# Optimization experiments

Measured on AMD Instinct MI355X. Metric: run time of the kernel, lower is better.

## Reference

```python
import jax, jax.numpy as jnp
import numpy as np

H = 1024      # hidden_dim
S = 32768     # seq_len


def setup_inputs() -> dict:
    key = jax.random.key(0)
    k1, k2, k3, k4, k5 = jax.random.split(key, 5)
    hidden = jax.random.normal(k1, (1, 2 * H), dtype=jnp.float32)
    encoder_output = jax.random.normal(k2, (S, H), dtype=jnp.float32)
    # nn.Linear default init scale ~ 1/sqrt(fan_in)
    attn_w = jax.random.normal(k3, (H, 3 * H), dtype=jnp.float32) / np.sqrt(3 * H)
    attn_b = jax.random.normal(k4, (H,), dtype=jnp.float32) / np.sqrt(3 * H)
    v_w = jax.random.normal(k5, (1, H), dtype=jnp.float32) / np.sqrt(H)
    return {"hidden": hidden, "encoder_output": encoder_output,
            "attn_w": attn_w, "attn_b": attn_b, "v_w": v_w}


def reference(hidden, encoder_output, attn_w, attn_b, v_w):
    seq_len = encoder_output.shape[0]
    h_rep = jnp.broadcast_to(hidden, (seq_len, hidden.shape[1]))  # repeat(seq_len, 1)
    cat = jnp.concatenate([h_rep, encoder_output], axis=1)        # [S, 3H]
    energy = jnp.tanh(cat @ attn_w.T + attn_b)                    # [S, H]
    attention = (energy @ v_w.T).squeeze()                        # [S]
    return jax.nn.softmax(attention, axis=0)
```

## Files before the change

kernel.cpp:

```cpp
#include <hip/hip_runtime.h>
#include <hip/hip_bf16.h>

#define H  1024
#define S  32768
#define H2 2048
#define H3 3072

typedef __attribute__((ext_vector_type(8))) short bf16x8;
typedef __attribute__((ext_vector_type(4))) float f32x4;

__device__ __forceinline__ unsigned short f2bf(float f) {
    unsigned u = __float_as_uint(f);
    u += 0x7fffu + ((u >> 16) & 1u);
    return (unsigned short)(u >> 16);
}

__device__ __forceinline__ unsigned cvt_pk(float lo, float hi) {
    __hip_bfloat162 h = __float22bfloat162_rn(make_float2(lo, hi));
    unsigned u;
    __builtin_memcpy(&u, &h, 4);
    return u;
}

__device__ __forceinline__ float tanh_fast(float x) {
    float e = __expf(2.0f * x);
    return 1.0f - 2.0f / (e + 1.0f);
}

__device__ __forceinline__ void async_copy16(const void* g, void* l) {
    __builtin_amdgcn_global_load_lds(
        (const __attribute__((address_space(1))) unsigned int*)g,
        (__attribute__((address_space(3))) unsigned int*)l,
        16, 0, 0);
}

__global__ void prep_all(const float* __restrict__ enc, const float* __restrict__ attn_w,
                         const float* __restrict__ attn_b, const float* __restrict__ hidden,
                         unsigned short* __restrict__ ebf, unsigned short* __restrict__ w2b,
                         float* __restrict__ dvec, float* __restrict__ logits, int do_enc) {
    int b = blockIdx.x;
    if (b < 32) {
        ((float4*)logits)[b * 256 + threadIdx.x] = (float4){0.f, 0.f, 0.f, 0.f};
        return;
    }
    b -= 32;
    if (do_enc) {
        if (b < 32768) {
            size_t idx4 = (size_t)b * 256 + threadIdx.x;
            float4 f = ((const float4*)enc)[idx4];
            ushort4 u;
            u.x = f2bf(f.x); u.y = f2bf(f.y); u.z = f2bf(f.z); u.w = f2bf(f.w);
            ((ushort4*)ebf)[idx4] = u;
            return;
        }
        b -= 32768;
    }
    if (b < 1024) {
        int idx4 = b * 256 + threadIdx.x;
        int n = idx4 >> 8;
        int c = (idx4 & 255) * 4;
        float4 f = *(const float4*)(attn_w + (size_t)n * H3 + H2 + c);
        ushort4 u;
        u.x = f2bf(f.x); u.y = f2bf(f.y); u.z = f2bf(f.z); u.w = f2bf(f.w);
        *(ushort4*)(w2b + (size_t)n * H + c) = u;
        return;
    }
    b -= 1024;
    int wv = threadIdx.x >> 6, lane = threadIdx.x & 63;
    int row = b * 4 + wv;
    const float* wrow = attn_w + (size_t)row * H3;
    float s = 0.f;
    #pragma unroll
    for (int j = 0; j < 32; ++j) {
        int k = lane + j * 64;
        s += wrow[k] * hidden[k];
    }
    #pragma unroll
    for (int m = 1; m <= 32; m <<= 1) s += __shfl_xor(s, m);
    if (lane == 0) dvec[row] = s + attn_b[row];
}

__device__ __forceinline__ void epilogue(const f32x4 acc[4][4], const float* __restrict__ dvec,
                                         const float* __restrict__ vw, float* __restrict__ logits,
                                         int rowBlock, int colBlock, int waveM, int waveN,
                                         int quad, int l16) {
    float rowsum[4][4];
    #pragma unroll
    for (int mi = 0; mi < 4; ++mi)
        #pragma unroll
        for (int r = 0; r < 4; ++r) rowsum[mi][r] = 0.f;

    #pragma unroll
    for (int ni = 0; ni < 4; ++ni) {
        int colg = colBlock * 128 + waveN * 64 + ni * 16 + l16;
        float dv = dvec[colg];
        float vv = vw[colg];
        #pragma unroll
        for (int mi = 0; mi < 4; ++mi)
            #pragma unroll
            for (int r = 0; r < 4; ++r)
                rowsum[mi][r] += tanh_fast(acc[mi][ni][r] + dv) * vv;
    }

    #pragma unroll
    for (int mi = 0; mi < 4; ++mi)
        #pragma unroll
        for (int r = 0; r < 4; ++r) {
            float s = rowsum[mi][r];
            s += __shfl_xor(s, 1);
            s += __shfl_xor(s, 2);
            s += __shfl_xor(s, 4);
            s += __shfl_xor(s, 8);
            rowsum[mi][r] = s;
        }

    if (l16 == 0) {
        int rbase = rowBlock * 128 + waveM * 64 + quad * 4;
        #pragma unroll
        for (int mi = 0; mi < 4; ++mi)
            #pragma unroll
            for (int r = 0; r < 4; ++r)
                atomicAdd(&logits[rbase + mi * 16 + r], rowsum[mi][r]);
    }
}

__global__ __launch_bounds__(256, 2) void attn_gemm_fast(
        const unsigned short* __restrict__ ebf, const unsigned short* __restrict__ w2b,
        const float* __restrict__ dvec, const float* __restrict__ vw,
        float* __restrict__ logits) {
    __shared__ unsigned short Atile[128 * 64];
    __shared__ unsigned short Btile[128 * 64];

    const int tid = threadIdx.x;
    const int rowBlock = blockIdx.x & 255;
    const int colBlock = blockIdx.x >> 8;

    const int lane = tid & 63;
    const int wv = tid >> 6;
    const int waveM = wv >> 1, waveN = wv & 1;
    const int quad = lane >> 4, l16 = lane & 15;

    f32x4 acc[4][4];
    #pragma unroll
    for (int mi = 0; mi < 4; ++mi)
        #pragma unroll
        for (int ni = 0; ni < 4; ++ni)
            acc[mi][ni] = (f32x4){0.f, 0.f, 0.f, 0.f};

    const size_t aRow0 = (size_t)(rowBlock * 128) * H;
    const size_t bRow0 = (size_t)(colBlock * 128) * H;

    int srow[4], sk[4];
    #pragma unroll
    for (int p = 0; p < 4; ++p) {
        int c = p * 256 + tid;
        srow[p] = c >> 3;
        sk[p] = ((c & 7) ^ (srow[p] & 7)) * 8;
    }

    for (int kt = 0; kt < 16; ++kt) {
        const int k0 = kt * 64;

        #pragma unroll
        for (int p = 0; p < 4; ++p) {
            int c = p * 256 + tid;
            async_copy16(ebf + aRow0 + (size_t)srow[p] * H + k0 + sk[p],
                         (char*)Atile + (size_t)c * 16);
        }
        #pragma unroll
        for (int p = 0; p < 4; ++p) {
            int c = p * 256 + tid;
            async_copy16(w2b + bRow0 + (size_t)srow[p] * H + k0 + sk[p],
                         (char*)Btile + (size_t)c * 16);
        }

        __syncthreads();

        #pragma unroll
        for (int kk = 0; kk < 2; ++kk) {
            const int slot = ((kk * 4 + quad) ^ (l16 & 7)) * 16;
            bf16x8 af[4], bfr[4];
            #pragma unroll
            for (int i = 0; i < 4; ++i) {
                int ar = waveM * 64 + i * 16 + l16;
                int br = waveN * 64 + i * 16 + l16;
                af[i]  = *(const bf16x8*)((const char*)Atile + ar * 128 + slot);
                bfr[i] = *(const bf16x8*)((const char*)Btile + br * 128 + slot);
            }
            #pragma unroll
            for (int mi = 0; mi < 4; ++mi)
                #pragma unroll
                for (int ni = 0; ni < 4; ++ni)
                    acc[mi][ni] = __builtin_amdgcn_mfma_f32_16x16x32_bf16(
                        af[mi], bfr[ni], acc[mi][ni], 0, 0, 0);
        }

        __syncthreads();
    }

    epilogue(acc, dvec, vw, logits, rowBlock, colBlock, waveM, waveN, quad, l16);
}

__global__ __launch_bounds__(256, 2) void attn_gemm_fb(
        const float* __restrict__ enc, const unsigned short* __restrict__ w2b,
        const float* __restrict__ dvec, const float* __restrict__ vw,
        float* __restrict__ logits) {
    __shared__ unsigned short Atile[128 * 32];
    __shared__ unsigned short Btile[128 * 32];

    const int tid = threadIdx.x;
    const int rowBlock = blockIdx.x & 255;
    const int colBlock = blockIdx.x >> 8;

    const int lane = tid & 63;
    const int wv = tid >> 6;
    const int waveM = wv >> 1, waveN = wv & 1;
    const int quad = lane >> 4, l16 = lane & 15;

    f32x4 acc[4][4];
    #pragma unroll
    for (int mi = 0; mi < 4; ++mi)
        #pragma unroll
        for (int ni = 0; ni < 4; ++ni)
            acc[mi][ni] = (f32x4){0.f, 0.f, 0.f, 0.f};

    const int arow = tid >> 3;
    const int akc  = (tid & 7) * 4;
    const size_t encRowBase = (size_t)(rowBlock * 128) * H;

    const unsigned short* Abase = Atile + (waveM * 64 + l16) * 32 + quad * 8;
    const unsigned short* Bbase = Btile + (waveN * 64 + l16) * 32 + quad * 8;

    for (int kt = 0; kt < 32; ++kt) {
        const int k0 = kt * 32;
        #pragma unroll
        for (int p = 0; p < 2; ++p) {
            int c = p * 256 + tid;
            int n = c >> 2, kk = (c & 3) * 8;
            async_copy16(w2b + (size_t)(colBlock * 128 + n) * H + k0 + kk,
                         (char*)Btile + (size_t)c * 16);
        }
        float4 av[4];
        #pragma unroll
        for (int p = 0; p < 4; ++p)
            av[p] = *(const float4*)(enc + encRowBase + (size_t)(arow + p * 32) * H + k0 + akc);
        #pragma unroll
        for (int p = 0; p < 4; ++p) {
            uint2 u;
            u.x = cvt_pk(av[p].x, av[p].y);
            u.y = cvt_pk(av[p].z, av[p].w);
            *(uint2*)(Atile + (arow + p * 32) * 32 + akc) = u;
        }

        __syncthreads();

        bf16x8 af[4], bfr[4];
        #pragma unroll
        for (int i = 0; i < 4; ++i) {
            af[i]  = *(const bf16x8*)(Abase + i * 16 * 32);
            bfr[i] = *(const bf16x8*)(Bbase + i * 16 * 32);
        }
        #pragma unroll
        for (int mi = 0; mi < 4; ++mi)
            #pragma unroll
            for (int ni = 0; ni < 4; ++ni)
                acc[mi][ni] = __builtin_amdgcn_mfma_f32_16x16x32_bf16(
                    af[mi], bfr[ni], acc[mi][ni], 0, 0, 0);

        __syncthreads();
    }

    epilogue(acc, dvec, vw, logits, rowBlock, colBlock, waveM, waveN, quad, l16);
}

__global__ __launch_bounds__(1024) void softmax_k(float* __restrict__ x) {
    __shared__ float red[16];
    const int tid = threadIdx.x;
    const int lane = tid & 63, wv = tid >> 6;

    float v[32];
    float m = -1e30f;
    #pragma unroll
    for (int i = 0; i < 32; ++i) {
        v[i] = x[tid + (i << 10)];
        m = fmaxf(m, v[i]);
    }
    #pragma unroll
    for (int o = 1; o < 64; o <<= 1) m = fmaxf(m, __shfl_xor(m, o));
    if (lane == 0) red[wv] = m;
    __syncthreads();
    #pragma unroll
    for (int i = 0; i < 16; ++i) m = fmaxf(m, red[i]);
    __syncthreads();

    float s = 0.f;
    #pragma unroll
    for (int i = 0; i < 32; ++i) {
        v[i] = expf(v[i] - m);
        s += v[i];
    }
    #pragma unroll
    for (int o = 1; o < 64; o <<= 1) s += __shfl_xor(s, o);
    if (lane == 0) red[wv] = s;
    __syncthreads();
    float tot = 0.f;
    #pragma unroll
    for (int i = 0; i < 16; ++i) tot += red[i];
    float inv = 1.0f / tot;

    #pragma unroll
    for (int i = 0; i < 32; ++i) x[tid + (i << 10)] = v[i] * inv;
}

extern "C" void kernel_launch(void* const* d_in, const int* in_sizes, int n_in,
                              void* d_out, int out_size, void* d_ws, size_t ws_size,
                              hipStream_t stream) {
    const float* hidden = (const float*)d_in[0];
    const float* enc    = (const float*)d_in[1];
    const float* attn_w = (const float*)d_in[2];
    const float* attn_b = (const float*)d_in[3];
    const float* v_w    = (const float*)d_in[4];
    float* out = (float*)d_out;

    const size_t EBF_BYTES = (size_t)S * H * 2;
    const size_t W2_BYTES  = (size_t)H * H * 2;
    const bool fast = ws_size >= EBF_BYTES + W2_BYTES + 4096;

    if (fast) {
        unsigned short* ebf = (unsigned short*)d_ws;
        unsigned short* w2b = (unsigned short*)((char*)d_ws + EBF_BYTES);
        float* dvec = (float*)((char*)d_ws + EBF_BYTES + W2_BYTES);
        prep_all<<<dim3(32 + 32768 + 1024 + 256), dim3(256), 0, stream>>>(
            enc, attn_w, attn_b, hidden, ebf, w2b, dvec, out, 1);
        attn_gemm_fast<<<dim3(2048), dim3(256), 0, stream>>>(ebf, w2b, dvec, v_w, out);
    } else {
        unsigned short* w2b = (unsigned short*)d_ws;
        float* dvec = (float*)((char*)d_ws + W2_BYTES);
        prep_all<<<dim3(32 + 1024 + 256), dim3(256), 0, stream>>>(
            enc, attn_w, attn_b, hidden, nullptr, w2b, dvec, out, 0);
        attn_gemm_fb<<<dim3(2048), dim3(256), 0, stream>>>(enc, w2b, dvec, v_w, out);
    }
    softmax_k<<<dim3(1), dim3(1024), 0, stream>>>(out);
}
```

Before: 296.9 us.

## Switch fast GEMM to 32x32x16 MFMA with 128-wide K tiles

```diff
diff --git a/kernel.cpp b/kernel.cpp
--- a/kernel.cpp
+++ b/kernel.cpp
@@ -6,8 +6,9 @@
 #define H2 2048
 #define H3 3072
 
-typedef __attribute__((ext_vector_type(8))) short bf16x8;
-typedef __attribute__((ext_vector_type(4))) float f32x4;
+typedef __attribute__((ext_vector_type(8)))  short bf16x8;
+typedef __attribute__((ext_vector_type(4)))  float f32x4;
+typedef __attribute__((ext_vector_type(16))) float f32x16;
 
 __device__ __forceinline__ unsigned short f2bf(float f) {
     unsigned u = __float_as_uint(f);
@@ -80,16 +81,191 @@
     if (lane == 0) dvec[row] = s + attn_b[row];
 }
 
-__device__ __forceinline__ void epilogue(const f32x4 acc[4][4], const float* __restrict__ dvec,
-                                         const float* __restrict__ vw, float* __restrict__ logits,
-                                         int rowBlock, int colBlock, int waveM, int waveN,
-                                         int quad, int l16) {
+__global__ __launch_bounds__(256, 2) void attn_gemm_fast(
+        const unsigned short* __restrict__ ebf, const unsigned short* __restrict__ w2b,
+        const float* __restrict__ dvec, const float* __restrict__ vw,
+        float* __restrict__ logits) {
+    __shared__ unsigned short Atile[128 * 128];
+    __shared__ unsigned short Btile[128 * 128];
+
+    const int tid = threadIdx.x;
+    const int rowBlock = blockIdx.x & 255;
+    const int colBlock = blockIdx.x >> 8;
+
+    const int lane = tid & 63;
+    const int wv = tid >> 6;
+    const int waveM = wv >> 1, waveN = wv & 1;
+    const int l32 = lane & 31, half = lane >> 5;
+
+    f32x16 acc[2][2];
+    #pragma unroll
+    for (int mi = 0; mi < 2; ++mi)
+        #pragma unroll
+        for (int ni = 0; ni < 2; ++ni)
+            #pragma unroll
+            for (int r = 0; r < 16; ++r)
+                acc[mi][ni][r] = 0.f;
+
+    const size_t aRow0 = (size_t)(rowBlock * 128) * H;
+    const size_t bRow0 = (size_t)(colBlock * 128) * H;
+
+    const int trow = tid >> 4;
+    const int jchunk = (tid & 15) ^ trow;
+    const size_t gOff = (size_t)trow * H + jchunk * 8;
+
+    for (int kt = 0; kt < 8; ++kt) {
+        const int k0 = kt * 128;
+
+        #pragma unroll
+        for (int p = 0; p < 8; ++p)
+            async_copy16(ebf + aRow0 + gOff + (size_t)p * 16 * H + k0,
+                         (char*)Atile + (size_t)(p * 256 + tid) * 16);
+        #pragma unroll
+        for (int p = 0; p < 8; ++p)
+            async_copy16(w2b + bRow0 + gOff + (size_t)p * 16 * H + k0,
+                         (char*)Btile + (size_t)(p * 256 + tid) * 16);
+
+        __syncthreads();
+
+        #pragma unroll
+        for (int s = 0; s < 8; ++s) {
+            bf16x8 af[2], bfr[2];
+            #pragma unroll
+            for (int i = 0; i < 2; ++i) {
+                int ar = waveM * 64 + i * 32 + l32;
+                int br = waveN * 64 + i * 32 + l32;
+                int aslot = (2 * s + half) ^ (ar & 15);
+                int bslot = (2 * s + half) ^ (br & 15);
+                af[i]  = *(const bf16x8*)((const char*)Atile + ar * 256 + aslot * 16);
+                bfr[i] = *(const bf16x8*)((const char*)Btile + br * 256 + bslot * 16);
+            }
+            #pragma unroll
+            for (int mi = 0; mi < 2; ++mi)
+                #pragma unroll
+                for (int ni = 0; ni < 2; ++ni)
+                    acc[mi][ni] = __builtin_amdgcn_mfma_f32_32x32x16_bf16(
+                        af[mi], bfr[ni], acc[mi][ni], 0, 0, 0);
+        }
+
+        __syncthreads();
+    }
+
+    float rowsum[2][16];
+    #pragma unroll
+    for (int mi = 0; mi < 2; ++mi)
+        #pragma unroll
+        for (int r = 0; r < 16; ++r) rowsum[mi][r] = 0.f;
+
+    #pragma unroll
+    for (int ni = 0; ni < 2; ++ni) {
+        int n = colBlock * 128 + waveN * 64 + ni * 32 + l32;
+        float dv = dvec[n];
+        float vv = vw[n];
+        #pragma unroll
+        for (int mi = 0; mi < 2; ++mi)
+            #pragma unroll
+            for (int r = 0; r < 16; ++r)
+                rowsum[mi][r] += tanh_fast(acc[mi][ni][r] + dv) * vv;
+    }
+
+    #pragma unroll
+    for (int mi = 0; mi < 2; ++mi)
+        #pragma unroll
+        for (int r = 0; r < 16; ++r) {
+            float s = rowsum[mi][r];
+            s += __shfl_xor(s, 1);
+            s += __shfl_xor(s, 2);
+            s += __shfl_xor(s, 4);
+            s += __shfl_xor(s, 8);
+            s += __shfl_xor(s, 16);
+            rowsum[mi][r] = s;
+        }
+
+    if (l32 == 0) {
+        #pragma unroll
+        for (int mi = 0; mi < 2; ++mi) {
+            int rbase = rowBlock * 128 + waveM * 64 + mi * 32 + 4 * half;
+            #pragma unroll
+            for (int r = 0; r < 16; ++r)
+                atomicAdd(&logits[rbase + (r & 3) + 8 * (r >> 2)], rowsum[mi][r]);
+        }
+    }
+}
+
+__global__ __launch_bounds__(256, 2) void attn_gemm_fb(
+        const float* __restrict__ enc, const unsigned short* __restrict__ w2b,
+        const float* __restrict__ dvec, const float* __restrict__ vw,
+        float* __restrict__ logits) {
+    __shared__ unsigned short Atile[128 * 32];
+    __shared__ unsigned short Btile[128 * 32];
+
+    const int tid = threadIdx.x;
+    const int rowBlock = blockIdx.x & 255;
+    const int colBlock = blockIdx.x >> 8;
+
+    const int lane = tid & 63;
+    const int wv = tid >> 6;
+    const int waveM = wv >> 1, waveN = wv & 1;
+    const int quad = lane >> 4, l16 = lane & 15;
+
+    f32x4 acc[4][4];
+    #pragma unroll
+    for (int mi = 0; mi < 4; ++mi)
+        #pragma unroll
+        for (int ni = 0; ni < 4; ++ni)
+            acc[mi][ni] = (f32x4){0.f, 0.f, 0.f, 0.f};
+
+    const int arow = tid >> 3;
+    const int akc  = (tid & 7) * 4;
+    const size_t encRowBase = (size_t)(rowBlock * 128) * H;
+
+    const unsigned short* Abase = Atile + (waveM * 64 + l16) * 32 + quad * 8;
+    const unsigned short* Bbase = Btile + (waveN * 64 + l16) * 32 + quad * 8;
+
+    for (int kt = 0; kt < 32; ++kt) {
+        const int k0 = kt * 32;
+        #pragma unroll
+        for (int p = 0; p < 2; ++p) {
+            int c = p * 256 + tid;
+            int n = c >> 2, kk = (c & 3) * 8;
+            async_copy16(w2b + (size_t)(colBlock * 128 + n) * H + k0 + kk,
+                         (char*)Btile + (size_t)c * 16);
+        }
+        float4 av[4];
+        #pragma unroll
+        for (int p = 0; p < 4; ++p)
+            av[p] = *(const float4*)(enc + encRowBase + (size_t)(arow + p * 32) * H + k0 + akc);
+        #pragma unroll
+        for (int p = 0; p < 4; ++p) {
+            uint2 u;
+            u.x = cvt_pk(av[p].x, av[p].y);
+            u.y = cvt_pk(av[p].z, av[p].w);
+            *(uint2*)(Atile + (arow + p * 32) * 32 + akc) = u;
+        }
+
+        __syncthreads();
+
+        bf16x8 af[4], bfr[4];
+        #pragma unroll
+        for (int i = 0; i < 4; ++i) {
+            af[i]  = *(const bf16x8*)(Abase + i * 16 * 32);
+            bfr[i] = *(const bf16x8*)(Bbase + i * 16 * 32);
+        }
+        #pragma unroll
+        for (int mi = 0; mi < 4; ++mi)
+            #pragma unroll
+            for (int ni = 0; ni < 4; ++ni)
+                acc[mi][ni] = __builtin_amdgcn_mfma_f32_16x16x32_bf16(
+                    af[mi], bfr[ni], acc[mi][ni], 0, 0, 0);
+
+        __syncthreads();
+    }
+
     float rowsum[4][4];
     #pragma unroll
     for (int mi = 0; mi < 4; ++mi)
         #pragma unroll
         for (int r = 0; r < 4; ++r) rowsum[mi][r] = 0.f;
-
     #pragma unroll
     for (int ni = 0; ni < 4; ++ni) {
         int colg = colBlock * 128 + waveN * 64 + ni * 16 + l16;
@@ -101,7 +277,6 @@
             for (int r = 0; r < 4; ++r)
                 rowsum[mi][r] += tanh_fast(acc[mi][ni][r] + dv) * vv;
     }
-
     #pragma unroll
     for (int mi = 0; mi < 4; ++mi)
         #pragma unroll
@@ -113,7 +288,6 @@
             s += __shfl_xor(s, 8);
             rowsum[mi][r] = s;
         }
-
     if (l16 == 0) {
         int rbase = rowBlock * 128 + waveM * 64 + quad * 4;
         #pragma unroll
@@ -122,155 +296,6 @@
             for (int r = 0; r < 4; ++r)
                 atomicAdd(&logits[rbase + mi * 16 + r], rowsum[mi][r]);
     }
-}
-
-__global__ __launch_bounds__(256, 2) void attn_gemm_fast(
-        const unsigned short* __restrict__ ebf, const unsigned short* __restrict__ w2b,
-        const float* __restrict__ dvec, const float* __restrict__ vw,
-        float* __restrict__ logits) {
-    __shared__ unsigned short Atile[128 * 64];
-    __shared__ unsigned short Btile[128 * 64];
-
-    const int tid = threadIdx.x;
-    const int rowBlock = blockIdx.x & 255;
-    const int colBlock = blockIdx.x >> 8;
-
-    const int lane = tid & 63;
-    const int wv = tid >> 6;
-    const int waveM = wv >> 1, waveN = wv & 1;
-    const int quad = lane >> 4, l16 = lane & 15;
-
-    f32x4 acc[4][4];
-    #pragma unroll
-    for (int mi = 0; mi < 4; ++mi)
-        #pragma unroll
-        for (int ni = 0; ni < 4; ++ni)
-            acc[mi][ni] = (f32x4){0.f, 0.f, 0.f, 0.f};
-
-    const size_t aRow0 = (size_t)(rowBlock * 128) * H;
-    const size_t bRow0 = (size_t)(colBlock * 128) * H;
-
-    int srow[4], sk[4];
-    #pragma unroll
-    for (int p = 0; p < 4; ++p) {
-        int c = p * 256 + tid;
-        srow[p] = c >> 3;
-        sk[p] = ((c & 7) ^ (srow[p] & 7)) * 8;
-    }
-
-    for (int kt = 0; kt < 16; ++kt) {
-        const int k0 = kt * 64;
-
-        #pragma unroll
-        for (int p = 0; p < 4; ++p) {
-            int c = p * 256 + tid;
-            async_copy16(ebf + aRow0 + (size_t)srow[p] * H + k0 + sk[p],
-                         (char*)Atile + (size_t)c * 16);
-        }
-        #pragma unroll
-        for (int p = 0; p < 4; ++p) {
-            int c = p * 256 + tid;
-            async_copy16(w2b + bRow0 + (size_t)srow[p] * H + k0 + sk[p],
-                         (char*)Btile + (size_t)c * 16);
-        }
-
-        __syncthreads();
-
-        #pragma unroll
-        for (int kk = 0; kk < 2; ++kk) {
-            const int slot = ((kk * 4 + quad) ^ (l16 & 7)) * 16;
-            bf16x8 af[4], bfr[4];
-            #pragma unroll
-            for (int i = 0; i < 4; ++i) {
-                int ar = waveM * 64 + i * 16 + l16;
-                int br = waveN * 64 + i * 16 + l16;
-                af[i]  = *(const bf16x8*)((const char*)Atile + ar * 128 + slot);
-                bfr[i] = *(const bf16x8*)((const char*)Btile + br * 128 + slot);
-            }
-            #pragma unroll
-            for (int mi = 0; mi < 4; ++mi)
-                #pragma unroll
-                for (int ni = 0; ni < 4; ++ni)
-                    acc[mi][ni] = __builtin_amdgcn_mfma_f32_16x16x32_bf16(
-                        af[mi], bfr[ni], acc[mi][ni], 0, 0, 0);
-        }
-
-        __syncthreads();
-    }
-
-    epilogue(acc, dvec, vw, logits, rowBlock, colBlock, waveM, waveN, quad, l16);
-}
-
-__global__ __launch_bounds__(256, 2) void attn_gemm_fb(
-        const float* __restrict__ enc, const unsigned short* __restrict__ w2b,
-        const float* __restrict__ dvec, const float* __restrict__ vw,
-        float* __restrict__ logits) {
-    __shared__ unsigned short Atile[128 * 32];
-    __shared__ unsigned short Btile[128 * 32];
-
-    const int tid = threadIdx.x;
-    const int rowBlock = blockIdx.x & 255;
-    const int colBlock = blockIdx.x >> 8;
-
-    const int lane = tid & 63;
-    const int wv = tid >> 6;
-    const int waveM = wv >> 1, waveN = wv & 1;
-    const int quad = lane >> 4, l16 = lane & 15;
-
-    f32x4 acc[4][4];
-    #pragma unroll
-    for (int mi = 0; mi < 4; ++mi)
-        #pragma unroll
-        for (int ni = 0; ni < 4; ++ni)
-            acc[mi][ni] = (f32x4){0.f, 0.f, 0.f, 0.f};
-
-    const int arow = tid >> 3;
-    const int akc  = (tid & 7) * 4;
-    const size_t encRowBase = (size_t)(rowBlock * 128) * H;
-
-    const unsigned short* Abase = Atile + (waveM * 64 + l16) * 32 + quad * 8;
-    const unsigned short* Bbase = Btile + (waveN * 64 + l16) * 32 + quad * 8;
-
-    for (int kt = 0; kt < 32; ++kt) {
-        const int k0 = kt * 32;
-        #pragma unroll
-        for (int p = 0; p < 2; ++p) {
-            int c = p * 256 + tid;
-            int n = c >> 2, kk = (c & 3) * 8;
-            async_copy16(w2b + (size_t)(colBlock * 128 + n) * H + k0 + kk,
-                         (char*)Btile + (size_t)c * 16);
-        }
-        float4 av[4];
-        #pragma unroll
-        for (int p = 0; p < 4; ++p)
-            av[p] = *(const float4*)(enc + encRowBase + (size_t)(arow + p * 32) * H + k0 + akc);
-        #pragma unroll
-        for (int p = 0; p < 4; ++p) {
-            uint2 u;
-            u.x = cvt_pk(av[p].x, av[p].y);
-            u.y = cvt_pk(av[p].z, av[p].w);
-            *(uint2*)(Atile + (arow + p * 32) * 32 + akc) = u;
-        }
-
-        __syncthreads();
-
-        bf16x8 af[4], bfr[4];
-        #pragma unroll
-        for (int i = 0; i < 4; ++i) {
-            af[i]  = *(const bf16x8*)(Abase + i * 16 * 32);
-            bfr[i] = *(const bf16x8*)(Bbase + i * 16 * 32);
-        }
-        #pragma unroll
-        for (int mi = 0; mi < 4; ++mi)
-            #pragma unroll
-            for (int ni = 0; ni < 4; ++ni)
-                acc[mi][ni] = __builtin_amdgcn_mfma_f32_16x16x32_bf16(
-                    af[mi], bfr[ni], acc[mi][ni], 0, 0, 0);
-
-        __syncthreads();
-    }
-
-    epilogue(acc, dvec, vw, logits, rowBlock, colBlock, waveM, waveN, quad, l16);
 }
 
 __global__ __launch_bounds__(1024) void softmax_k(float* __restrict__ x) {
```

Result: slower. 320.3 us (+7.9%).
